# Performance work log

Measured on AMD Instinct MI355X. Metric: run time of the kernel, lower is better.

Reference implementation:

```python
import jax, jax.numpy as jnp
import numpy as np


def setup_inputs() -> dict:
    key = jax.random.key(0)
    k1, k2, k3 = jax.random.split(key, 3)
    N, C, V, T, K = 32, 64, 25, 1024, 3
    x = jax.random.normal(k1, (N, C, V, T), dtype=jnp.float32)
    # grouped 1x1 conv weight: per node v, maps C -> K*C. torch weight (C*K*V, C, 1, 1)
    W = jax.random.normal(k2, (V, K * C, C), dtype=jnp.float32) * 0.05
    # adjacency buffer A[k, w, v] (src node w -> dst node v, partition k)
    A = jax.random.uniform(k3, (K, V, V), dtype=jnp.float32)
    return {"x": x, "W": W, "A": A}


def reference(x, W, A):
    # x: [N, C, V, T]; W: [V, K*C, C]; A: [K, V, V]
    N, C, V, T = x.shape
    K = A.shape[0]
    # permute(0,2,1,3): [N, V, C, T]; grouped 1x1 conv == per-node matmul C -> K*C
    y = jnp.einsum('ncvt,voc->nvot', x, W)          # [N, V, K*C, T]
    # view (N, V, C*K, T) with output-channel layout o = c*K + k -> split to (C, K)
    y = y.reshape(N, V, C, K, T)                     # [N, V(src=w), C, K, T]
    # einsum('kwv,nckwt->ncvt')
    out = jnp.einsum('kwv,nwckt->ncvt', A, y)        # [N, C, V, T]
    return out
```

## Files before the change

kernel.cpp:

```cpp
#include <hip/hip_runtime.h>

#define Nn 32
#define Cc 64
#define Vv 25
#define Tt 1024

typedef __attribute__((ext_vector_type(4))) float f32x4;
typedef __attribute__((ext_vector_type(8))) short bf16x8;
typedef __attribute__((ext_vector_type(4))) unsigned short u16x4;

__device__ __forceinline__ unsigned short f2bf(float f) {
    union { float f; unsigned u; } a; a.f = f;
    unsigned u = a.u;
    u += 0x7fff + ((u >> 16) & 1);
    return (unsigned short)(u >> 16);
}

__device__ __forceinline__ void gl_lds16(const unsigned short* g, unsigned short* l) {
    __builtin_amdgcn_global_load_lds(
        (const __attribute__((address_space(1))) unsigned int*)g,
        (__attribute__((address_space(3))) unsigned int*)l, 16, 0, 0);
}


__global__ __launch_bounds__(256) void prep_fused(
        const float* __restrict__ x, const float* __restrict__ W,
        const float* __restrict__ A, unsigned short* __restrict__ xb,
        unsigned short* __restrict__ Weff) {
    int bid = blockIdx.x;
    if (bid < Vv * Vv) {
        int v = bid / Vv;
        int w = bid - v * Vv;
        float a0 = A[(0 * Vv + w) * Vv + v];
        float a1 = A[(1 * Vv + w) * Vv + v];
        float a2 = A[(2 * Vv + w) * Vv + v];
        const float* Wb = W + (size_t)w * 192 * 64;
        unsigned short* o = Weff + (size_t)(v * Vv + w) * 4096;
        int c  = threadIdx.x >> 2;
        int c0 = (threadIdx.x & 3) * 16;
        #pragma unroll
        for (int i = 0; i < 16; ++i) {
            int cp = c0 + i;
            float val = a0 * Wb[(c * 3 + 0) * 64 + cp]
                      + a1 * Wb[(c * 3 + 1) * 64 + cp]
                      + a2 * Wb[(c * 3 + 2) * 64 + cp];
            int jl = cp >> 3;
            o[c * 64 + ((jl ^ (c & 7)) << 3) + (cp & 7)] = f2bf(val);
        }
        return;
    }
    int pid = bid - Vv * Vv;
    int n = pid / (Vv * 4);
    int rem = pid - n * (Vv * 4);
    int w = rem >> 2;
    int sl = rem & 3;

    int tid = threadIdx.x;
    int wq = tid >> 6;
    int l  = tid & 63;
    int quad = l >> 4, m = l & 15;

    const float* xw = x + ((size_t)n * Cc * Vv + w) * Tt + sl * 256 + wq * 64 + m;
    unsigned short* dst = xb +
        ((((size_t)(n * Vv + w) * 4 + sl) * 2048) + (size_t)wq * 512 + l) * 8;

    #pragma unroll
    for (int kc = 0; kc < 2; ++kc) {
        float vals[4][8];
        #pragma unroll
        for (int kk = 0; kk < 8; ++kk) {
            int cp = (kc * 4 + quad) * 8 + kk;
            const float* row = xw + (size_t)cp * (Vv * Tt);
            #pragma unroll
            for (int ni = 0; ni < 4; ++ni)
                vals[ni][kk] = __builtin_nontemporal_load(row + ni * 16);
        }
        #pragma unroll
        for (int ni = 0; ni < 4; ++ni) {
            bf16x8 o;
            #pragma unroll
            for (int kk = 0; kk < 8; ++kk) o[kk] = (short)f2bf(vals[ni][kk]);
            *(bf16x8*)&dst[(size_t)(kc * 256 + ni * 64) * 8] = o;
        }
    }
}

__global__ __launch_bounds__(256, 2) void gc_fast(
        const unsigned short* __restrict__ xb,
        const unsigned short* __restrict__ Weff,
        float* __restrict__ out) {
    __shared__ __align__(16) unsigned short wa[8][4096];

    int bid = blockIdx.x;
    int xcd = bid & 7;
    int lid = bid >> 3;
    int v = lid % Vv;
    int s = lid / Vv;
    int slice = (xcd << 4) + s;
    int n  = slice >> 2;
    int sl = slice & 3;
    int t0 = sl << 8;

    int tid = threadIdx.x;
    int lane = tid & 63, wv = tid >> 6;
    int m = lane & 15, quad = lane >> 4;

    const unsigned short* wg = Weff + (size_t)v * (Vv * 4096);
    const unsigned short* xbase = xb + ((size_t)(n * Vv * 4 + sl)) * 2048 * 8;

    int coff0 = ((quad)     ^ (m & 7)) << 3;
    int coff1 = ((4 + quad) ^ (m & 7)) << 3;
    int arow[4];
    #pragma unroll
    for (int mi = 0; mi < 4; ++mi) arow[mi] = (mi * 16 + m) * 64;
    int boff[8];
    #pragma unroll
    for (int q = 0; q < 8; ++q) boff[q] = ((wv * 8 + q) * 64 + lane) * 8;

    f32x4 acc[4][4];
    #pragma unroll
    for (int i = 0; i < 4; ++i)
        #pragma unroll
        for (int j = 0; j < 4; ++j)
            acc[i][j] = (f32x4){0.f, 0.f, 0.f, 0.f};

    bf16x8 b0v[8], b1v[8], b2v[8];

#define SB __builtin_amdgcn_sched_barrier(0)
#define VMCNT(N_) asm volatile("s_waitcnt vmcnt(" #N_ ")" ::: "memory")

#define ISSUE_A(WBUF, w_) do { \
    const unsigned short* s_ = wg + (size_t)(w_) * 4096 + tid * 8; \
    gl_lds16(s_,        &wa[WBUF][tid * 8]); \
    gl_lds16(s_ + 2048, &wa[WBUF][2048 + tid * 8]); \
} while (0)

#define ISSUE_B(BN, w_) do { \
    const unsigned short* xw_ = xbase + (size_t)(w_) * 65536; \
    _Pragma("unroll") \
    for (int q_ = 0; q_ < 8; ++q_) \
        BN[q_] = *(const bf16x8*)(xw_ + boff[q_]); \
} while (0)

#define COMP(RBUF, BC) do { \
    const unsigned short* cur_ = &wa[RBUF][0]; \
    bf16x8 af_[8]; \
    _Pragma("unroll") \
    for (int mi_ = 0; mi_ < 4; ++mi_) { \
        af_[mi_]     = *(const bf16x8*)(cur_ + arow[mi_] + coff0); \
        af_[mi_ + 4] = *(const bf16x8*)(cur_ + arow[mi_] + coff1); \
    } \
    __builtin_amdgcn_s_setprio(1); \
    _Pragma("unroll") \
    for (int mi_ = 0; mi_ < 4; ++mi_) \
        _Pragma("unroll") \
        for (int ni_ = 0; ni_ < 4; ++ni_) \
            acc[mi_][ni_] = __builtin_amdgcn_mfma_f32_16x16x32_bf16( \
                af_[mi_], BC[ni_], acc[mi_][ni_], 0, 0, 0); \
    _Pragma("unroll") \
    for (int mi_ = 0; mi_ < 4; ++mi_) \
        _Pragma("unroll") \
        for (int ni_ = 0; ni_ < 4; ++ni_) \
            acc[mi_][ni_] = __builtin_amdgcn_mfma_f32_16x16x32_bf16( \
                af_[mi_ + 4], BC[ni_ + 4], acc[mi_][ni_], 0, 0, 0); \
    __builtin_amdgcn_s_setprio(0); \
} while (0)

#define DSTEP(R0, R1, W4, W5, C0, C1, I2, I3, w_, N3, N6) do { \
    ISSUE_B(I2, (w_) + 2); \
    ISSUE_A(W4, (w_) + 4); \
    ISSUE_A(W5, (w_) + 5); \
    SB; VMCNT(N3); SB; \
    __builtin_amdgcn_s_barrier(); \
    SB; \
    COMP(R0, C0); \
    SB; \
    ISSUE_B(I3, (w_) + 3); \
    SB; VMCNT(N6); SB; \
    COMP(R1, C1); \
    SB; \
} while (0)

    ISSUE_B(b0v, 0);
    ISSUE_B(b1v, 1);
    ISSUE_A(0, 0);
    ISSUE_A(1, 1);
    ISSUE_A(2, 2);
    ISSUE_A(3, 3);
    SB;

    DSTEP(0, 1, 4, 5, b0v, b1v, b2v, b0v,  0, 16, 20);
    DSTEP(2, 3, 6, 7, b2v, b0v, b1v, b2v,  2, 24, 20);
    DSTEP(4, 5, 0, 1, b1v, b2v, b0v, b1v,  4, 24, 20);
    DSTEP(6, 7, 2, 3, b0v, b1v, b2v, b0v,  6, 24, 20);
    DSTEP(0, 1, 4, 5, b2v, b0v, b1v, b2v,  8, 24, 20);
    DSTEP(2, 3, 6, 7, b1v, b2v, b0v, b1v, 10, 24, 20);
    DSTEP(4, 5, 0, 1, b0v, b1v, b2v, b0v, 12, 24, 20);
    DSTEP(6, 7, 2, 3, b2v, b0v, b1v, b2v, 14, 24, 20);
    DSTEP(0, 1, 4, 5, b1v, b2v, b0v, b1v, 16, 24, 20);
    DSTEP(2, 3, 6, 7, b0v, b1v, b2v, b0v, 18, 24, 20);

    ISSUE_B(b1v, 22);
    ISSUE_A(0, 24);
    SB; VMCNT(22); SB;
    __builtin_amdgcn_s_barrier();
    SB;
    COMP(4, b2v);
    SB;
    ISSUE_B(b2v, 23);
    SB; VMCNT(18); SB;
    COMP(5, b0v);
    SB;

    ISSUE_B(b0v, 24);
    SB; VMCNT(18); SB;
    __builtin_amdgcn_s_barrier();
    SB;
    COMP(6, b1v);
    SB; VMCNT(10); SB;
    COMP(7, b2v);
    SB;

    VMCNT(0);
    SB;
    __builtin_amdgcn_s_barrier();
    SB;
    COMP(0, b0v);

#undef DSTEP
#undef COMP
#undef ISSUE_B
#undef ISSUE_A
#undef VMCNT
#undef SB

    float* og = out + ((size_t)n * Cc * Vv + v) * Tt + t0 + wv * 64 + m;
    #pragma unroll
    for (int mi = 0; mi < 4; ++mi)
        #pragma unroll
        for (int r = 0; r < 4; ++r) {
            int c = mi * 16 + quad * 4 + r;
            float* orow = og + (size_t)c * Vv * Tt;
            #pragma unroll
            for (int ni = 0; ni < 4; ++ni)
                __builtin_nontemporal_store(acc[mi][ni][r], &orow[ni * 16]);
        }
}


__global__ __launch_bounds__(256) void weff_prep_plain(
        const float* __restrict__ W, const float* __restrict__ A,
        unsigned short* __restrict__ Weff) {
    int v = blockIdx.x / Vv;
    int w = blockIdx.x - v * Vv;
    float a0 = A[(0 * Vv + w) * Vv + v];
    float a1 = A[(1 * Vv + w) * Vv + v];
    float a2 = A[(2 * Vv + w) * Vv + v];
    const float* Wb = W + (size_t)w * 192 * 64;
    unsigned short* o = Weff + (size_t)(v * Vv + w) * 4096;
    int e0 = threadIdx.x * 16;
    #pragma unroll
    for (int i = 0; i < 16; ++i) {
        int e = e0 + i;
        int c = e >> 6, cp = e & 63;
        float val = a0 * Wb[(c * 3 + 0) * 64 + cp]
                  + a1 * Wb[(c * 3 + 1) * 64 + cp]
                  + a2 * Wb[(c * 3 + 2) * 64 + cp];
        o[e] = f2bf(val);
    }
}

__global__ __launch_bounds__(256, 2) void gc_plain(
        const float* __restrict__ x, const unsigned short* __restrict__ Weff,
        float* __restrict__ out) {
    __shared__ __align__(16) unsigned short xs[256 * 72];
    __shared__ __align__(16) unsigned short wa[64 * 72];
    int bid = blockIdx.x;
    int xcd = bid & 7;
    int lid = bid >> 3;
    int v, s;
    if (lid < 13 * 16) { v = lid % 13;            s = lid / 13; }
    else { int l2 = lid - 13 * 16; v = 13 + l2 % 12; s = l2 / 12; }
    int slice = (xcd << 4) + s;
    int n  = slice >> 2;
    int t0 = (slice & 3) << 8;
    int tid  = threadIdx.x;
    int lane = tid & 63;
    int wv   = tid >> 6;
    int m    = lane & 15;
    int quad = lane >> 4;
    int cc = tid & 7;
    int tt = tid >> 3;
    f32x4 acc[4][4];
    #pragma unroll
    for (int i = 0; i < 4; ++i)
        #pragma unroll
        for (int j = 0; j < 4; ++j)
            acc[i][j] = (f32x4){0.f, 0.f, 0.f, 0.f};
    const float* xg = x + (size_t)n * Cc * Vv * Tt + t0 + tt * 4;
    const bf16x8* wg = (const bf16x8*)(Weff + (size_t)v * Vv * 4096);
    for (int w = 0; w < Vv; ++w) {
        if (w) __syncthreads();
        #pragma unroll
        for (int r = 0; r < 2; ++r) {
            int q = r * 256 + tid;
            int c = q >> 3, b = q & 7;
            *(bf16x8*)&wa[c * 72 + b * 8] = wg[w * 512 + q];
        }
        {
            bf16x8 rows[8];
            #pragma unroll
            for (int i = 0; i < 8; ++i) {
                int cp = cc * 8 + i;
                const float* p = xg + ((size_t)cp * Vv + w) * Tt;
                float4 f0 = *(const float4*)p;
                float4 f1 = *(const float4*)(p + 128);
                rows[0][i] = (short)f2bf(f0.x); rows[1][i] = (short)f2bf(f0.y);
                rows[2][i] = (short)f2bf(f0.z); rows[3][i] = (short)f2bf(f0.w);
                rows[4][i] = (short)f2bf(f1.x); rows[5][i] = (short)f2bf(f1.y);
                rows[6][i] = (short)f2bf(f1.z); rows[7][i] = (short)f2bf(f1.w);
            }
            #pragma unroll
            for (int j = 0; j < 4; ++j) {
                *(bf16x8*)&xs[(tt * 4 + j) * 72 + cc * 8]       = rows[j];
                *(bf16x8*)&xs[(128 + tt * 4 + j) * 72 + cc * 8] = rows[4 + j];
            }
        }
        __syncthreads();
        #pragma unroll
        for (int kc = 0; kc < 2; ++kc) {
            int ko = kc * 32 + quad * 8;
            bf16x8 afr[4], bfr[4];
            #pragma unroll
            for (int mi = 0; mi < 4; ++mi)
                afr[mi] = *(const bf16x8*)&wa[(mi * 16 + m) * 72 + ko];
            #pragma unroll
            for (int ni = 0; ni < 4; ++ni)
                bfr[ni] = *(const bf16x8*)&xs[(wv * 64 + ni * 16 + m) * 72 + ko];
            #pragma unroll
            for (int mi = 0; mi < 4; ++mi)
                #pragma unroll
                for (int ni = 0; ni < 4; ++ni)
                    acc[mi][ni] = __builtin_amdgcn_mfma_f32_16x16x32_bf16(
                        afr[mi], bfr[ni], acc[mi][ni], 0, 0, 0);
        }
    }
    float* og = out + ((size_t)n * Cc * Vv + v) * Tt + t0 + wv * 64 + m;
    #pragma unroll
    for (int mi = 0; mi < 4; ++mi)
        #pragma unroll
        for (int r = 0; r < 4; ++r) {
            int c = mi * 16 + quad * 4 + r;
            float* orow = og + (size_t)c * Vv * Tt;
            #pragma unroll
            for (int ni = 0; ni < 4; ++ni)
                orow[ni * 16] = acc[mi][ni][r];
        }
}

extern "C" void kernel_launch(void* const* d_in, const int* in_sizes, int n_in,
                              void* d_out, int out_size, void* d_ws, size_t ws_size,
                              hipStream_t stream) {
    const float* x = (const float*)d_in[0];
    const float* W = (const float*)d_in[1];
    const float* A = (const float*)d_in[2];
    float* out = (float*)d_out;

    const size_t xb_elems   = (size_t)Nn * Vv * Tt * 64;
    const size_t weff_elems = (size_t)Vv * Vv * 4096;
    const size_t need = (xb_elems + weff_elems) * sizeof(unsigned short);

    if (ws_size >= need) {
        unsigned short* xb   = (unsigned short*)d_ws;
        unsigned short* Weff = xb + xb_elems;
        prep_fused<<<dim3(Vv * Vv + Nn * Vv * 4), dim3(256), 0, stream>>>(x, W, A, xb, Weff);
        gc_fast<<<dim3(3200), dim3(256), 0, stream>>>(xb, Weff, out);
    } else {
        unsigned short* Weff = (unsigned short*)d_ws;
        weff_prep_plain<<<dim3(Vv * Vv), dim3(256), 0, stream>>>(W, A, Weff);
        gc_plain<<<dim3(3200), dim3(256), 0, stream>>>(x, Weff, out);
    }
}
```

Measured before the change: 503.1 us.

## Shrink LDS weight ring to 4 buffers and register-prefetch A fragments

```diff
diff --git a/kernel.cpp b/kernel.cpp
--- a/kernel.cpp
+++ b/kernel.cpp
@@ -89,7 +89,7 @@
         const unsigned short* __restrict__ xb,
         const unsigned short* __restrict__ Weff,
         float* __restrict__ out) {
-    __shared__ __align__(16) unsigned short wa[8][4096];
+    __shared__ __align__(16) unsigned short wa[4][4096];
 
     int bid = blockIdx.x;
     int xcd = bid & 7;
@@ -125,6 +125,7 @@
             acc[i][j] = (f32x4){0.f, 0.f, 0.f, 0.f};
 
     bf16x8 b0v[8], b1v[8], b2v[8];
+    bf16x8 afA[8], afB[8];
 
 #define SB __builtin_amdgcn_sched_barrier(0)
 #define VMCNT(N_) asm volatile("s_waitcnt vmcnt(" #N_ ")" ::: "memory")
@@ -142,93 +143,89 @@
         BN[q_] = *(const bf16x8*)(xw_ + boff[q_]); \
 } while (0)
 
-#define COMP(RBUF, BC) do { \
+#define LDREAD(AF, RBUF) do { \
     const unsigned short* cur_ = &wa[RBUF][0]; \
-    bf16x8 af_[8]; \
     _Pragma("unroll") \
     for (int mi_ = 0; mi_ < 4; ++mi_) { \
-        af_[mi_]     = *(const bf16x8*)(cur_ + arow[mi_] + coff0); \
-        af_[mi_ + 4] = *(const bf16x8*)(cur_ + arow[mi_] + coff1); \
+        AF[mi_]     = *(const bf16x8*)(cur_ + arow[mi_] + coff0); \
+        AF[mi_ + 4] = *(const bf16x8*)(cur_ + arow[mi_] + coff1); \
     } \
+} while (0)
+
+#define COMP(AF, BC) do { \
     __builtin_amdgcn_s_setprio(1); \
     _Pragma("unroll") \
     for (int mi_ = 0; mi_ < 4; ++mi_) \
         _Pragma("unroll") \
         for (int ni_ = 0; ni_ < 4; ++ni_) \
             acc[mi_][ni_] = __builtin_amdgcn_mfma_f32_16x16x32_bf16( \
-                af_[mi_], BC[ni_], acc[mi_][ni_], 0, 0, 0); \
+                AF[mi_], BC[ni_], acc[mi_][ni_], 0, 0, 0); \
     _Pragma("unroll") \
     for (int mi_ = 0; mi_ < 4; ++mi_) \
         _Pragma("unroll") \
         for (int ni_ = 0; ni_ < 4; ++ni_) \
             acc[mi_][ni_] = __builtin_amdgcn_mfma_f32_16x16x32_bf16( \
-                af_[mi_ + 4], BC[ni_ + 4], acc[mi_][ni_], 0, 0, 0); \
+                AF[mi_ + 4], BC[ni_ + 4], acc[mi_][ni_], 0, 0, 0); \
     __builtin_amdgcn_s_setprio(0); \
 } while (0)
 
-#define DSTEP(R0, R1, W4, W5, C0, C1, I2, I3, w_, N3, N6) do { \
-    ISSUE_B(I2, (w_) + 2); \
-    ISSUE_A(W4, (w_) + 4); \
-    ISSUE_A(W5, (w_) + 5); \
-    SB; VMCNT(N3); SB; \
+#define STEP(AFc, AFn, WB, RB, BC, BN, w_) do { \
+    ISSUE_A(WB, (w_) + 2); \
+    ISSUE_B(BN, (w_) + 2); \
+    SB; VMCNT(18); SB; \
     __builtin_amdgcn_s_barrier(); \
     SB; \
-    COMP(R0, C0); \
+    COMP(AFc, BC); \
+    LDREAD(AFn, RB); \
     SB; \
-    ISSUE_B(I3, (w_) + 3); \
-    SB; VMCNT(N6); SB; \
-    COMP(R1, C1); \
-    SB; \
-} while (0)
-
+} while (0)
+
+    ISSUE_A(0, 0);
+    ISSUE_A(1, 1);
     ISSUE_B(b0v, 0);
     ISSUE_B(b1v, 1);
-    ISSUE_A(0, 0);
-    ISSUE_A(1, 1);
-    ISSUE_A(2, 2);
-    ISSUE_A(3, 3);
-    SB;
-
-    DSTEP(0, 1, 4, 5, b0v, b1v, b2v, b0v,  0, 16, 20);
-    DSTEP(2, 3, 6, 7, b2v, b0v, b1v, b2v,  2, 24, 20);
-    DSTEP(4, 5, 0, 1, b1v, b2v, b0v, b1v,  4, 24, 20);
-    DSTEP(6, 7, 2, 3, b0v, b1v, b2v, b0v,  6, 24, 20);
-    DSTEP(0, 1, 4, 5, b2v, b0v, b1v, b2v,  8, 24, 20);
-    DSTEP(2, 3, 6, 7, b1v, b2v, b0v, b1v, 10, 24, 20);
-    DSTEP(4, 5, 0, 1, b0v, b1v, b2v, b0v, 12, 24, 20);
-    DSTEP(6, 7, 2, 3, b2v, b0v, b1v, b2v, 14, 24, 20);
-    DSTEP(0, 1, 4, 5, b1v, b2v, b0v, b1v, 16, 24, 20);
-    DSTEP(2, 3, 6, 7, b0v, b1v, b2v, b0v, 18, 24, 20);
-
-    ISSUE_B(b1v, 22);
-    ISSUE_A(0, 24);
-    SB; VMCNT(22); SB;
+    SB; VMCNT(16); SB;
     __builtin_amdgcn_s_barrier();
     SB;
-    COMP(4, b2v);
-    SB;
-    ISSUE_B(b2v, 23);
-    SB; VMCNT(18); SB;
-    COMP(5, b0v);
-    SB;
-
-    ISSUE_B(b0v, 24);
-    SB; VMCNT(18); SB;
+    LDREAD(afA, 0);
+    SB;
+
+    STEP(afA, afB, 2, 1, b0v, b2v,  0);
+    STEP(afB, afA, 3, 2, b1v, b0v,  1);
+    STEP(afA, afB, 0, 3, b2v, b1v,  2);
+    STEP(afB, afA, 1, 0, b0v, b2v,  3);
+    STEP(afA, afB, 2, 1, b1v, b0v,  4);
+    STEP(afB, afA, 3, 2, b2v, b1v,  5);
+    STEP(afA, afB, 0, 3, b0v, b2v,  6);
+    STEP(afB, afA, 1, 0, b1v, b0v,  7);
+    STEP(afA, afB, 2, 1, b2v, b1v,  8);
+    STEP(afB, afA, 3, 2, b0v, b2v,  9);
+    STEP(afA, afB, 0, 3, b1v, b0v, 10);
+    STEP(afB, afA, 1, 0, b2v, b1v, 11);
+    STEP(afA, afB, 2, 1, b0v, b2v, 12);
+    STEP(afB, afA, 3, 2, b1v, b0v, 13);
+    STEP(afA, afB, 0, 3, b2v, b1v, 14);
+    STEP(afB, afA, 1, 0, b0v, b2v, 15);
+    STEP(afA, afB, 2, 1, b1v, b0v, 16);
+    STEP(afB, afA, 3, 2, b2v, b1v, 17);
+    STEP(afA, afB, 0, 3, b0v, b2v, 18);
+    STEP(afB, afA, 1, 0, b1v, b0v, 19);
+    STEP(afA, afB, 2, 1, b2v, b1v, 20);
+    STEP(afB, afA, 3, 2, b0v, b2v, 21);
+    STEP(afA, afB, 0, 3, b1v, b0v, 22);
+    SB; VMCNT(8); SB;
     __builtin_amdgcn_s_barrier();
     SB;
-    COMP(6, b1v);
-    SB; VMCNT(10); SB;
-    COMP(7, b2v);
-    SB;
-
+    COMP(afB, b2v);
+    LDREAD(afA, 0);
+    SB;
     VMCNT(0);
     SB;
-    __builtin_amdgcn_s_barrier();
-    SB;
-    COMP(0, b0v);
-
-#undef DSTEP
+    COMP(afA, b0v);
+
+#undef STEP
 #undef COMP
+#undef LDREAD
 #undef ISSUE_B
 #undef ISSUE_A
 #undef VMCNT
```

Result: faster. 492.3 us (median of 2 runs) (-2.2%).
